# Kernel optimization log

Hardware: AMD Instinct MI355X
Metric: run time of the kernel (lower is better)

Reference implementation:

```python
import jax, jax.numpy as jnp
import numpy as np

NUM_EXPERTS = 8
TOP_K = 2


def setup_inputs() -> dict:
    key = jax.random.key(0)
    k0, k1, k2, k3, k4 = jax.random.split(key, 5)
    sl, bs, hs, ffn = 2048, 2, 512, 2048
    T = sl * bs
    x = jax.random.normal(k0, (sl, bs, hs), jnp.float32)
    expert_weights = jax.random.uniform(k1, (T, TOP_K), jnp.float32)
    expert_indices = jax.random.randint(k2, (T, TOP_K), 0, NUM_EXPERTS)
    # per-expert MLP params (ParallelGroupedMLP, 'regular' mlp_type)
    w1 = jax.random.normal(k3, (NUM_EXPERTS, hs, ffn), jnp.float32) * (hs ** -0.5)
    w2 = jax.random.normal(k4, (NUM_EXPERTS, ffn, hs), jnp.float32) * (ffn ** -0.5)
    return dict(x=x, expert_weights=expert_weights, expert_indices=expert_indices, w1=w1, w2=w2)


def reference(x, expert_weights, expert_indices, w1, w2):
    """Dropless MoE: sort assignments by expert, gather tokens, grouped MLP,
    scatter-combine with top-k router weights (megablocks gather/scatter semantics)."""
    in_shape = x.shape
    hs = in_shape[-1]
    x_flat = x.reshape(-1, hs)                 # [T, hs]
    T = x_flat.shape[0]
    flat_ids = expert_indices.reshape(-1)      # [T*k] expert id per assignment
    order = jnp.argsort(flat_ids)              # indices: assignment order sorted by expert
    bin_ids = flat_ids[order]                  # expert id per sorted slot
    token_ids = order // TOP_K                 # source token per sorted slot
    xg = x_flat[token_ids]                     # gather: [T*k, hs]
    # grouped GEMM: fixed small loop over experts, mask-select per slot
    y = jnp.zeros_like(xg)
    for e in range(NUM_EXPERTS):
        h = jax.nn.gelu(xg @ w1[e], approximate=False)   # [T*k, ffn]
        y = jnp.where((bin_ids == e)[:, None], h @ w2[e], y)
    # scatter-combine: out[token] += weight[assignment] * y[slot]
    w = expert_weights.reshape(-1)[order][:, None]       # [T*k, 1]
    out = jnp.zeros((T, hs), x.dtype).at[token_ids].add(w * y)
    return out.reshape(in_shape)
```

## Files before the change

kernel.cpp:

```cpp
#include <hip/hip_runtime.h>
#include <stdint.h>

#define T_TOK 4096
#define KTOP  2
#define HS    512
#define FFN   2048
#define NE    8
#define NA    (T_TOK*KTOP)
#define MT    128
#define BK    64
#define MT_MAX 72
#define SLOT_CAP (MT_MAX*MT)
#define PSTR 68
#define NB_G1 1152

#define MB_ (1024ull*1024ull)
#define WS_OFF   1024u
#define WS_MEXP  1088u
#define WS_SLOTS 2048u
#define WS_INV   40960u
#define WS_XB   (1*MB_)
#define WS_W1T  (5*MB_)
#define WS_W2T  (21*MB_)
#define WS_HB   (37*MB_)
#define WS_YPB0 (73*MB_)
#define WS_YPB1 (82*MB_)
#define WS_NEED (91*MB_)

typedef short bf16x8 __attribute__((ext_vector_type(8)));
typedef float f32x4  __attribute__((ext_vector_type(4)));

__device__ __forceinline__ unsigned short f2bf(float f) {
    unsigned u = __builtin_bit_cast(unsigned, f);
    u += 0x7fffu + ((u >> 16) & 1u);
    return (unsigned short)(u >> 16);
}
__device__ __forceinline__ float bf2f(unsigned short h) {
    return __builtin_bit_cast(float, (unsigned)h << 16);
}
__device__ __forceinline__ float gelu_fast(float x) {
    float x2 = x * x;
    float inner = fmaf(0.044715f * x2, x, x);
    float E = __expf(1.5957691216057308f * inner);
    return x - x / (1.0f + E);
}
__device__ __forceinline__ void gl_lds16(const void* g, void* l) {
    __builtin_amdgcn_global_load_lds(
        (const __attribute__((address_space(1))) unsigned int*)g,
        (__attribute__((address_space(3))) unsigned int*)l, 16, 0, 0);
}

__device__ __forceinline__ void transpose_cvt64(
    const float* __restrict__ src, unsigned short* __restrict__ dh,
    int R, int C, int e, int kb, int nb, int t, float (*tile)[65])
{
    const int k0 = kb * 64, n0 = nb * 64;
    #pragma unroll
    for (int q = 0; q < 4; ++q) {
        int f4 = t + q * 256;
        int kk = f4 >> 4, nn4 = f4 & 15;
        float4 v = *reinterpret_cast<const float4*>(
            &src[((size_t)e * R + k0 + kk) * C + n0 + nn4 * 4]);
        tile[kk][nn4 * 4 + 0] = v.x; tile[kk][nn4 * 4 + 1] = v.y;
        tile[kk][nn4 * 4 + 2] = v.z; tile[kk][nn4 * 4 + 3] = v.w;
    }
    __syncthreads();
    #pragma unroll
    for (int q = 0; q < 4; ++q) {
        int wid = t + q * 256;
        int nn = wid >> 4, kk4 = wid & 15;
        ushort4 o;
        o.x = f2bf(tile[kk4 * 4 + 0][nn]);
        o.y = f2bf(tile[kk4 * 4 + 1][nn]);
        o.z = f2bf(tile[kk4 * 4 + 2][nn]);
        o.w = f2bf(tile[kk4 * 4 + 3][nn]);
        *reinterpret_cast<ushort4*>(&dh[((size_t)e * C + n0 + nn) * R + k0 + kk4 * 4]) = o;
    }
}

__global__ void moe_prep1(const int* __restrict__ eidx,
                          int* slots, int* inv, int* offp, int* mexp,
                          const float* __restrict__ x, unsigned short* __restrict__ xb,
                          const float* __restrict__ w1, unsigned short* __restrict__ w1t)
{
    __shared__ float tile[64][65];
    const int bid = blockIdx.x, t = threadIdx.x;
    if (bid < 2048) {
        int i = bid * 256 + t;
        float4 v = reinterpret_cast<const float4*>(x)[i];
        uint2 p = { (unsigned)f2bf(v.x) | ((unsigned)f2bf(v.y) << 16),
                    (unsigned)f2bf(v.z) | ((unsigned)f2bf(v.w) << 16) };
        reinterpret_cast<uint2*>(xb)[i] = p;
    } else if (bid < 4096) {
        int lin = bid - 2048, e = lin >> 8, rem = lin & 255;
        transpose_cvt64(w1, w1t, HS, FFN, e, rem & 7, rem >> 3, t, tile);
    } else {
        __shared__ int hfull[NE], hpre[NE], elocal[256];
        __shared__ int off_l[NE + 1];
        const int f = bid - 4096;
        if (t < NE) { hfull[t] = 0; hpre[t] = 0; }
        __syncthreads();
        const int base = f * 256;
        for (int i = t; i < NA; i += 256) {
            int ee = eidx[i];
            atomicAdd(&hfull[ee], 1);
            if (i < base) atomicAdd(&hpre[ee], 1);
        }
        if (f < 32) elocal[t] = eidx[base + t];
        __syncthreads();
        if (t == 0) {
            int run = 0;
            for (int q = 0; q < NE; ++q) { off_l[q] = run; run += ((hfull[q] + MT - 1) / MT) * MT; }
            off_l[NE] = run;
        }
        __syncthreads();
        if (f < 32) {
            int a = base + t, e = elocal[t];
            int rank = 0;
            for (int j = 0; j < t; ++j) rank += (elocal[j] == e) ? 1 : 0;
            int s = off_l[e] + hpre[e] + rank;
            slots[s] = a;
            inv[a] = s;
        } else {
            for (int e = 0; e < NE; ++e)
                for (int s = off_l[e] + hfull[e] + t; s < off_l[e + 1]; s += 256)
                    slots[s] = -1;
            for (int s = off_l[NE] + t; s < SLOT_CAP; s += 256) slots[s] = -1;
            if (t <= NE) offp[t] = off_l[t];
            if (t < MT_MAX) {
                int m0 = t * MT, ee = 0;
                #pragma unroll
                for (int q = 0; q < NE; ++q)
                    if (m0 >= off_l[q] && m0 < off_l[q + 1]) ee = q;
                mexp[t] = ee;
            }
        }
    }
}

__global__ __launch_bounds__(256, 4) void moe_g1w2(
    const unsigned short* __restrict__ XB, const unsigned short* __restrict__ W1T,
    const int* __restrict__ offp, const int* __restrict__ mexp,
    const int* __restrict__ slots, unsigned short* __restrict__ HB,
    const float* __restrict__ w2, unsigned short* __restrict__ w2t)
{
    __shared__ __align__(16) char POOL[MT * PSTR * 4];
    __shared__ int srow[MT];
    const int t = threadIdx.x;

    if (blockIdx.x >= NB_G1) {
        int lin = blockIdx.x - NB_G1;
        int e = lin >> 8, rem = lin & 255;
        transpose_cvt64(w2, w2t, FFN, HS, e, rem & 31, rem >> 5, t,
                        reinterpret_cast<float(*)[65]>(POOL));
        return;
    }

    const int xcd = blockIdx.x & 7;
    const int part = blockIdx.x >> 3;
    const int mtg = part % 9;
    const int nt  = part / 9;
    const int mt  = xcd * 9 + mtg;
    if (mt * MT >= offp[NE]) return;
    const int e = mexp[mt];
    const int lane = t & 63, wv = t >> 6;

    short* As = (short*)POOL;
    short* Bs = (short*)(POOL + 16384);
    float* Pf = (float*)POOL;

    if (t < MT) { int s = slots[mt * MT + t]; srow[t] = (s < 0) ? 0 : (s >> 1); }
    __syncthreads();

    int baseA[4], baseB[4];
    #pragma unroll
    for (int q = 0; q < 4; ++q) {
        int i = wv * 4 + q;
        int row = i * 8 + (lane >> 3);
        int sg = (lane & 7) ^ (row & 7);
        baseA[q] = srow[row] * HS + sg * 8;
        baseB[q] = (e * FFN + nt * MT + row) * HS + sg * 8;
    }

    const int wm = wv >> 1, wn = wv & 1, q4 = lane >> 4, l15 = lane & 15;
    int offA[2][4], offB[2][4];
    #pragma unroll
    for (int m = 0; m < 4; ++m) {
        int r  = wm * 64 + m * 16 + l15;
        int rb = wn * 64 + m * 16 + l15;
        #pragma unroll
        for (int ks = 0; ks < 2; ++ks) {
            offA[ks][m] = r  * 128 + ((((ks << 2) | q4) ^ (r  & 7)) << 4);
            offB[ks][m] = rb * 128 + ((((ks << 2) | q4) ^ (rb & 7)) << 4);
        }
    }

    f32x4 acc[4][4];
    #pragma unroll
    for (int m = 0; m < 4; ++m)
        #pragma unroll
        for (int n = 0; n < 4; ++n) { f32x4 z = {0.f, 0.f, 0.f, 0.f}; acc[m][n] = z; }

    for (int kk = 0; kk < HS; kk += BK) {
        __syncthreads();
        #pragma unroll
        for (int q = 0; q < 4; ++q) {
            int i = wv * 4 + q;
            gl_lds16(XB  + baseA[q] + kk, (char*)As + i * 1024);
            gl_lds16(W1T + baseB[q] + kk, (char*)Bs + i * 1024);
        }
        __syncthreads();
        #pragma unroll
        for (int ks = 0; ks < 2; ++ks) {
            bf16x8 a[4], b[4];
            #pragma unroll
            for (int m = 0; m < 4; ++m) {
                a[m] = *(const bf16x8*)((const char*)As + offA[ks][m]);
                b[m] = *(const bf16x8*)((const char*)Bs + offB[ks][m]);
            }
            #pragma unroll
            for (int m = 0; m < 4; ++m)
                #pragma unroll
                for (int n = 0; n < 4; ++n)
                    acc[m][n] = __builtin_amdgcn_mfma_f32_16x16x32_bf16(a[m], b[n], acc[m][n], 0, 0, 0);
        }
    }

    #pragma unroll
    for (int half = 0; half < 2; ++half) {
        __syncthreads();
        if (wn == half) {
            #pragma unroll
            for (int m = 0; m < 4; ++m)
                #pragma unroll
                for (int n = 0; n < 4; ++n)
                    #pragma unroll
                    for (int j = 0; j < 4; ++j)
                        Pf[(wm * 64 + m * 16 + q4 * 4 + j) * PSTR + n * 16 + l15] = acc[m][n][j];
        }
        __syncthreads();
        #pragma unroll
        for (int q = 0; q < 4; ++q) {
            int seg = q * 256 + t, row = seg >> 3, c8 = (seg & 7) << 3;
            const float* p = Pf + row * PSTR + c8;
            float4 a = *(const float4*)p, b = *(const float4*)(p + 4);
            float va[8] = {a.x, a.y, a.z, a.w, b.x, b.y, b.z, b.w};
            bf16x8 ph;
            #pragma unroll
            for (int i = 0; i < 8; ++i) ph[i] = (short)f2bf(gelu_fast(va[i]));
            *(bf16x8*)(HB + (size_t)(mt * MT + row) * FFN + nt * MT + half * 64 + c8) = ph;
        }
    }
}

__global__ __launch_bounds__(256, 4) void moe_gemm2(
    const unsigned short* __restrict__ HB, const unsigned short* __restrict__ W2T,
    const int* __restrict__ offp, const int* __restrict__ mexp,
    unsigned short* __restrict__ YPB0, unsigned short* __restrict__ YPB1)
{
    const int xcd = blockIdx.x & 7;
    const int part = blockIdx.x >> 3;
    const int sub = part % 8;
    const int mtg = part / 8;
    const int mt  = xcd * 9 + mtg;
    const int nt  = sub >> 1, kpart = sub & 1;
    if (mt * MT >= offp[NE]) return;
    const int e = mexp[mt];
    const int t = threadIdx.x, lane = t & 63, wv = t >> 6;

    __shared__ __align__(16) char POOL[MT * PSTR * 4];
    short* As = (short*)POOL;
    short* Bs = (short*)(POOL + 16384);
    float* Pf = (float*)POOL;

    int baseA[4], baseB[4];
    #pragma unroll
    for (int q = 0; q < 4; ++q) {
        int i = wv * 4 + q;
        int row = i * 8 + (lane >> 3);
        int sg = (lane & 7) ^ (row & 7);
        baseA[q] = (mt * MT + row) * FFN + sg * 8;
        baseB[q] = (e * HS + nt * MT + row) * FFN + sg * 8;
    }

    const int wm = wv >> 1, wn = wv & 1, q4 = lane >> 4, l15 = lane & 15;
    int offA[2][4], offB[2][4];
    #pragma unroll
    for (int m = 0; m < 4; ++m) {
        int r  = wm * 64 + m * 16 + l15;
        int rb = wn * 64 + m * 16 + l15;
        #pragma unroll
        for (int ks = 0; ks < 2; ++ks) {
            offA[ks][m] = r  * 128 + ((((ks << 2) | q4) ^ (r  & 7)) << 4);
            offB[ks][m] = rb * 128 + ((((ks << 2) | q4) ^ (rb & 7)) << 4);
        }
    }

    f32x4 acc[4][4];
    #pragma unroll
    for (int m = 0; m < 4; ++m)
        #pragma unroll
        for (int n = 0; n < 4; ++n) { f32x4 z = {0.f, 0.f, 0.f, 0.f}; acc[m][n] = z; }

    const int k0 = kpart * (FFN / 2), k1 = k0 + FFN / 2;
    for (int kk = k0; kk < k1; kk += BK) {
        __syncthreads();
        #pragma unroll
        for (int q = 0; q < 4; ++q) {
            int i = wv * 4 + q;
            gl_lds16(HB  + baseA[q] + kk, (char*)As + i * 1024);
            gl_lds16(W2T + baseB[q] + kk, (char*)Bs + i * 1024);
        }
        __syncthreads();
        #pragma unroll
        for (int ks = 0; ks < 2; ++ks) {
            bf16x8 a[4], b[4];
            #pragma unroll
            for (int m = 0; m < 4; ++m) {
                a[m] = *(const bf16x8*)((const char*)As + offA[ks][m]);
                b[m] = *(const bf16x8*)((const char*)Bs + offB[ks][m]);
            }
            #pragma unroll
            for (int m = 0; m < 4; ++m)
                #pragma unroll
                for (int n = 0; n < 4; ++n)
                    acc[m][n] = __builtin_amdgcn_mfma_f32_16x16x32_bf16(a[m], b[n], acc[m][n], 0, 0, 0);
        }
    }

    unsigned short* YP = kpart ? YPB1 : YPB0;
    #pragma unroll
    for (int half = 0; half < 2; ++half) {
        __syncthreads();
        if (wn == half) {
            #pragma unroll
            for (int m = 0; m < 4; ++m)
                #pragma unroll
                for (int n = 0; n < 4; ++n)
                    #pragma unroll
                    for (int j = 0; j < 4; ++j)
                        Pf[(wm * 64 + m * 16 + q4 * 4 + j) * PSTR + n * 16 + l15] = acc[m][n][j];
        }
        __syncthreads();
        #pragma unroll
        for (int q = 0; q < 4; ++q) {
            int seg = q * 256 + t, row = seg >> 3, c8 = (seg & 7) << 3;
            const float* p = Pf + row * PSTR + c8;
            float4 a = *(const float4*)p, b = *(const float4*)(p + 4);
            float va[8] = {a.x, a.y, a.z, a.w, b.x, b.y, b.z, b.w};
            bf16x8 ph;
            #pragma unroll
            for (int i = 0; i < 8; ++i) ph[i] = (short)f2bf(va[i]);
            *(bf16x8*)(YP + (size_t)(mt * MT + row) * HS + nt * MT + half * 64 + c8) = ph;
        }
    }
}

__global__ void moe_combine2(const unsigned short* __restrict__ YPB0,
                             const unsigned short* __restrict__ YPB1,
                             const int* __restrict__ inv, const float* __restrict__ ew,
                             float* __restrict__ out) {
    int i = blockIdx.x * 256 + threadIdx.x;
    if (i >= T_TOK * HS / 8) return;
    int tk = i >> 6, c8 = (i & 63) << 3;
    int s0 = inv[2 * tk], s1 = inv[2 * tk + 1];
    float w0 = ew[2 * tk], w1 = ew[2 * tk + 1];
    bf16x8 a0 = *(const bf16x8*)(YPB0 + (size_t)s0 * HS + c8);
    bf16x8 b0 = *(const bf16x8*)(YPB1 + (size_t)s0 * HS + c8);
    bf16x8 a1 = *(const bf16x8*)(YPB0 + (size_t)s1 * HS + c8);
    bf16x8 b1 = *(const bf16x8*)(YPB1 + (size_t)s1 * HS + c8);
    float o[8];
    #pragma unroll
    for (int j = 0; j < 8; ++j)
        o[j] = w0 * (bf2f((unsigned short)a0[j]) + bf2f((unsigned short)b0[j]))
             + w1 * (bf2f((unsigned short)a1[j]) + bf2f((unsigned short)b1[j]));
    float4* d = reinterpret_cast<float4*>(out + (size_t)i * 8);
    d[0] = make_float4(o[0], o[1], o[2], o[3]);
    d[1] = make_float4(o[4], o[5], o[6], o[7]);
}

#define FB_BM 32
#define FB_BJ 128
#define FB_CK 256
#define FB_XSTR (FB_CK+4)
#define FB_HSTR (FB_BJ+4)

__device__ __forceinline__ float fb_gelu(float v) {
    return 0.5f * v * (1.0f + erff(v * 0.70710678118654752f));
}

__global__ void fb_init(int* cnt) { int i = threadIdx.x; if (i < NE) cnt[i] = 0; }

__global__ void fb_scatter(const int* __restrict__ eidx, int* cnt, int* bucket) {
    int a = blockIdx.x * 256 + threadIdx.x;
    if (a < NA) { int e = eidx[a]; int p = atomicAdd(&cnt[e], 1); bucket[e * NA + p] = a; }
}

__global__ __launch_bounds__(256, 1) void fb_fused(
    const float* __restrict__ x, const float* __restrict__ w1, const float* __restrict__ w2,
    const int* __restrict__ cnt, const int* __restrict__ bucket, float* __restrict__ ybuf)
{
    const int bid = blockIdx.x;
    const int e = bid & (NE - 1), tr = bid >> 3;
    const int n_e = cnt[e], rbase = tr * FB_BM;
    if (rbase >= n_e) return;
    const int t = threadIdx.x;
    __shared__ __align__(16) float Xc[FB_BM][FB_XSTR];
    __shared__ __align__(16) float Hsh[FB_BM][FB_HSTR];
    __shared__ int rowa[FB_BM];
    if (t < FB_BM) { int r = rbase + t; rowa[t] = (r < n_e) ? bucket[e * NA + r] : -1; }
    __syncthreads();
    const int cg = t & 15, rg = t >> 4, r0 = rg * 2;
    float yac[2][32];
    #pragma unroll
    for (int u = 0; u < 2; ++u)
        #pragma unroll
        for (int v = 0; v < 32; ++v) yac[u][v] = 0.0f;
    const float* w1e = w1 + (size_t)e * HS * FFN;
    const float* w2e = w2 + (size_t)e * FFN * HS;
    for (int jp = 0; jp < FFN; jp += FB_BJ) {
        float hac[2][8];
        #pragma unroll
        for (int u = 0; u < 2; ++u)
            #pragma unroll
            for (int v = 0; v < 8; ++v) hac[u][v] = 0.0f;
        for (int ic = 0; ic < HS; ic += FB_CK) {
            __syncthreads();
            #pragma unroll
            for (int q = 0; q < (FB_BM * FB_CK / 4) / 256; ++q) {
                int id = t + 256 * q, rr = id >> 6, c4 = id & 63;
                int a = rowa[rr];
                float4 val = make_float4(0.f, 0.f, 0.f, 0.f);
                if (a >= 0) val = *reinterpret_cast<const float4*>(x + (size_t)(a >> 1) * HS + ic + c4 * 4);
                *reinterpret_cast<float4*>(&Xc[rr][c4 * 4]) = val;
            }
            __syncthreads();
            const float* w1p = w1e + (size_t)ic * FFN + jp + cg * 8;
            #pragma unroll 2
            for (int i4 = 0; i4 < FB_CK; i4 += 4) {
                float4 xa = *reinterpret_cast<const float4*>(&Xc[r0][i4]);
                float4 xb = *reinterpret_cast<const float4*>(&Xc[r0 + 1][i4]);
                const float* wr0 = w1p + (size_t)i4 * FFN;
                #pragma unroll
                for (int ii = 0; ii < 4; ++ii) {
                    float4 wa = *reinterpret_cast<const float4*>(wr0 + (size_t)ii * FFN);
                    float4 wb = *reinterpret_cast<const float4*>(wr0 + (size_t)ii * FFN + 4);
                    float x0 = (ii == 0) ? xa.x : (ii == 1) ? xa.y : (ii == 2) ? xa.z : xa.w;
                    float x1 = (ii == 0) ? xb.x : (ii == 1) ? xb.y : (ii == 2) ? xb.z : xb.w;
                    hac[0][0] = fmaf(x0, wa.x, hac[0][0]); hac[0][1] = fmaf(x0, wa.y, hac[0][1]);
                    hac[0][2] = fmaf(x0, wa.z, hac[0][2]); hac[0][3] = fmaf(x0, wa.w, hac[0][3]);
                    hac[0][4] = fmaf(x0, wb.x, hac[0][4]); hac[0][5] = fmaf(x0, wb.y, hac[0][5]);
                    hac[0][6] = fmaf(x0, wb.z, hac[0][6]); hac[0][7] = fmaf(x0, wb.w, hac[0][7]);
                    hac[1][0] = fmaf(x1, wa.x, hac[1][0]); hac[1][1] = fmaf(x1, wa.y, hac[1][1]);
                    hac[1][2] = fmaf(x1, wa.z, hac[1][2]); hac[1][3] = fmaf(x1, wa.w, hac[1][3]);
                    hac[1][4] = fmaf(x1, wb.x, hac[1][4]); hac[1][5] = fmaf(x1, wb.y, hac[1][5]);
                    hac[1][6] = fmaf(x1, wb.z, hac[1][6]); hac[1][7] = fmaf(x1, wb.w, hac[1][7]);
                }
            }
        }
        #pragma unroll
        for (int u = 0; u < 2; ++u)
            #pragma unroll
            for (int v = 0; v < 8; ++v) Hsh[r0 + u][cg * 8 + v] = fb_gelu(hac[u][v]);
        __syncthreads();
        const float* w2p = w2e + (size_t)jp * HS + cg * 32;
        #pragma unroll 2
        for (int j = 0; j < FB_BJ; ++j) {
            float h0 = Hsh[r0][j], h1 = Hsh[r0 + 1][j];
            const float* wr = w2p + (size_t)j * HS;
            #pragma unroll
            for (int q = 0; q < 8; ++q) {
                float4 w4 = *reinterpret_cast<const float4*>(wr + q * 4);
                yac[0][q * 4 + 0] = fmaf(h0, w4.x, yac[0][q * 4 + 0]);
                yac[0][q * 4 + 1] = fmaf(h0, w4.y, yac[0][q * 4 + 1]);
                yac[0][q * 4 + 2] = fmaf(h0, w4.z, yac[0][q * 4 + 2]);
                yac[0][q * 4 + 3] = fmaf(h0, w4.w, yac[0][q * 4 + 3]);
                yac[1][q * 4 + 0] = fmaf(h1, w4.x, yac[1][q * 4 + 0]);
                yac[1][q * 4 + 1] = fmaf(h1, w4.y, yac[1][q * 4 + 1]);
                yac[1][q * 4 + 2] = fmaf(h1, w4.z, yac[1][q * 4 + 2]);
                yac[1][q * 4 + 3] = fmaf(h1, w4.w, yac[1][q * 4 + 3]);
            }
        }
    }
    #pragma unroll
    for (int u = 0; u < 2; ++u) {
        int a = rowa[r0 + u];
        if (a >= 0) {
            float* yp = ybuf + (size_t)a * HS + cg * 32;
            #pragma unroll
            for (int q = 0; q < 8; ++q) {
                float4 o = make_float4(yac[u][q * 4 + 0], yac[u][q * 4 + 1],
                                       yac[u][q * 4 + 2], yac[u][q * 4 + 3]);
                *reinterpret_cast<float4*>(yp + q * 4) = o;
            }
        }
    }
}

__global__ void fb_combine(const float* __restrict__ ybuf, const float* __restrict__ ew,
                           float* __restrict__ out) {
    int i = blockIdx.x * 256 + threadIdx.x;
    if (i >= T_TOK * HS / 4) return;
    int tk = i >> 7, c4 = i & 127;
    float wA = ew[2 * tk], wB = ew[2 * tk + 1];
    const float4* y4 = reinterpret_cast<const float4*>(ybuf);
    float4 a = y4[(size_t)(2 * tk) * (HS / 4) + c4];
    float4 b = y4[(size_t)(2 * tk + 1) * (HS / 4) + c4];
    float4 o;
    o.x = wA * a.x + wB * b.x; o.y = wA * a.y + wB * b.y;
    o.z = wA * a.z + wB * b.z; o.w = wA * a.w + wB * b.w;
    reinterpret_cast<float4*>(out)[i] = o;
}

extern "C" void kernel_launch(void* const* d_in, const int* in_sizes, int n_in,
                              void* d_out, int out_size, void* d_ws, size_t ws_size,
                              hipStream_t stream) {
    const float* x  = (const float*)d_in[0];
    const float* ew = (const float*)d_in[1];
    const int*   ei = (const int*)d_in[2];
    const float* w1 = (const float*)d_in[3];
    const float* w2 = (const float*)d_in[4];
    float* out = (float*)d_out;
    char* W = (char*)d_ws;

    if (ws_size < WS_NEED) {
        int* cnt = (int*)d_ws;
        int* bucket = cnt + 64;
        float* ybuf = (float*)(W + (1 << 19));
        fb_init<<<1, 64, 0, stream>>>(cnt);
        fb_scatter<<<NA / 256, 256, 0, stream>>>(ei, cnt, bucket);
        fb_fused<<<NE * (NA / FB_BM), 256, 0, stream>>>(x, w1, w2, cnt, bucket, ybuf);
        fb_combine<<<(T_TOK * HS / 4 + 255) / 256, 256, 0, stream>>>(ybuf, ew, out);
        return;
    }

    int* offp  = (int*)(W + WS_OFF);
    int* mexp  = (int*)(W + WS_MEXP);
    int* slots = (int*)(W + WS_SLOTS);
    int* inv   = (int*)(W + WS_INV);
    unsigned short* XB   = (unsigned short*)(W + WS_XB);
    unsigned short* W1T  = (unsigned short*)(W + WS_W1T);
    unsigned short* W2T  = (unsigned short*)(W + WS_W2T);
    unsigned short* HB   = (unsigned short*)(W + WS_HB);
    unsigned short* YPB0 = (unsigned short*)(W + WS_YPB0);
    unsigned short* YPB1 = (unsigned short*)(W + WS_YPB1);

    moe_prep1<<<4129, 256, 0, stream>>>(ei, slots, inv, offp, mexp, x, XB, w1, W1T);
    moe_g1w2<<<NB_G1 + 2048, 256, 0, stream>>>(XB, W1T, offp, mexp, slots, HB, w2, W2T);
    moe_gemm2<<<8 * 9 * 8, 256, 0, stream>>>(HB, W2T, offp, mexp, YPB0, YPB1);
    moe_combine2<<<(T_TOK * HS / 8) / 256, 256, 0, stream>>>(YPB0, YPB1, inv, ew, out);
}
```

Baseline: 96.66 us.

## Widen GEMM1 N-tile to 256 columns per block for better A reuse

```diff
diff --git a/kernel.cpp b/kernel.cpp
--- a/kernel.cpp
+++ b/kernel.cpp
@@ -12,7 +12,7 @@
 #define MT_MAX 72
 #define SLOT_CAP (MT_MAX*MT)
 #define PSTR 68
-#define NB_G1 1152
+#define NB_G1 576
 
 #define MB_ (1024ull*1024ull)
 #define WS_OFF   1024u
@@ -138,13 +138,13 @@
     }
 }
 
-__global__ __launch_bounds__(256, 4) void moe_g1w2(
+__global__ __launch_bounds__(256, 2) void moe_g1w2(
     const unsigned short* __restrict__ XB, const unsigned short* __restrict__ W1T,
     const int* __restrict__ offp, const int* __restrict__ mexp,
     const int* __restrict__ slots, unsigned short* __restrict__ HB,
     const float* __restrict__ w2, unsigned short* __restrict__ w2t)
 {
-    __shared__ __align__(16) char POOL[MT * PSTR * 4];
+    __shared__ __align__(16) char POOL[49152];
     __shared__ int srow[MT];
     const int t = threadIdx.x;
 
@@ -172,71 +172,83 @@
     if (t < MT) { int s = slots[mt * MT + t]; srow[t] = (s < 0) ? 0 : (s >> 1); }
     __syncthreads();
 
-    int baseA[4], baseB[4];
+    int baseA[4], baseB[8];
     #pragma unroll
     for (int q = 0; q < 4; ++q) {
         int i = wv * 4 + q;
         int row = i * 8 + (lane >> 3);
         int sg = (lane & 7) ^ (row & 7);
         baseA[q] = srow[row] * HS + sg * 8;
-        baseB[q] = (e * FFN + nt * MT + row) * HS + sg * 8;
+    }
+    #pragma unroll
+    for (int q = 0; q < 8; ++q) {
+        int j = wv * 8 + q;
+        int row = j * 8 + (lane >> 3);
+        int sg = (lane & 7) ^ (row & 7);
+        baseB[q] = (e * FFN + nt * 256 + row) * HS + sg * 8;
     }
 
     const int wm = wv >> 1, wn = wv & 1, q4 = lane >> 4, l15 = lane & 15;
-    int offA[2][4], offB[2][4];
+    int offA[2][4], offB[2][8];
     #pragma unroll
     for (int m = 0; m < 4; ++m) {
-        int r  = wm * 64 + m * 16 + l15;
-        int rb = wn * 64 + m * 16 + l15;
+        int r = wm * 64 + m * 16 + l15;
+        #pragma unroll
+        for (int ks = 0; ks < 2; ++ks)
+            offA[ks][m] = r * 128 + ((((ks << 2) | q4) ^ (r & 7)) << 4);
+    }
+    #pragma unroll
+    for (int n = 0; n < 8; ++n) {
+        int rb = wn * 128 + n * 16 + l15;
+        #pragma unroll
+        for (int ks = 0; ks < 2; ++ks)
+            offB[ks][n] = rb * 128 + ((((ks << 2) | q4) ^ (rb & 7)) << 4);
+    }
+
+    f32x4 acc[4][8];
+    #pragma unroll
+    for (int m = 0; m < 4; ++m)
+        #pragma unroll
+        for (int n = 0; n < 8; ++n) { f32x4 z = {0.f, 0.f, 0.f, 0.f}; acc[m][n] = z; }
+
+    for (int kk = 0; kk < HS; kk += BK) {
+        __syncthreads();
+        #pragma unroll
+        for (int q = 0; q < 4; ++q)
+            gl_lds16(XB + baseA[q] + kk, (char*)As + (wv * 4 + q) * 1024);
+        #pragma unroll
+        for (int q = 0; q < 8; ++q)
+            gl_lds16(W1T + baseB[q] + kk, (char*)Bs + (wv * 8 + q) * 1024);
+        __syncthreads();
         #pragma unroll
         for (int ks = 0; ks < 2; ++ks) {
-            offA[ks][m] = r  * 128 + ((((ks << 2) | q4) ^ (r  & 7)) << 4);
-            offB[ks][m] = rb * 128 + ((((ks << 2) | q4) ^ (rb & 7)) << 4);
-        }
-    }
-
-    f32x4 acc[4][4];
-    #pragma unroll
-    for (int m = 0; m < 4; ++m)
-        #pragma unroll
-        for (int n = 0; n < 4; ++n) { f32x4 z = {0.f, 0.f, 0.f, 0.f}; acc[m][n] = z; }
-
-    for (int kk = 0; kk < HS; kk += BK) {
-        __syncthreads();
-        #pragma unroll
-        for (int q = 0; q < 4; ++q) {
-            int i = wv * 4 + q;
-            gl_lds16(XB  + baseA[q] + kk, (char*)As + i * 1024);
-            gl_lds16(W1T + baseB[q] + kk, (char*)Bs + i * 1024);
-        }
-        __syncthreads();
-        #pragma unroll
-        for (int ks = 0; ks < 2; ++ks) {
-            bf16x8 a[4], b[4];
-            #pragma unroll
-            for (int m = 0; m < 4; ++m) {
+            bf16x8 a[4], b[8];
+            #pragma unroll
+            for (int m = 0; m < 4; ++m)
                 a[m] = *(const bf16x8*)((const char*)As + offA[ks][m]);
-                b[m] = *(const bf16x8*)((const char*)Bs + offB[ks][m]);
-            }
+            #pragma unroll
+            for (int n = 0; n < 8; ++n)
+                b[n] = *(const bf16x8*)((const char*)Bs + offB[ks][n]);
             #pragma unroll
             for (int m = 0; m < 4; ++m)
                 #pragma unroll
-                for (int n = 0; n < 4; ++n)
+                for (int n = 0; n < 8; ++n)
                     acc[m][n] = __builtin_amdgcn_mfma_f32_16x16x32_bf16(a[m], b[n], acc[m][n], 0, 0, 0);
         }
     }
 
     #pragma unroll
-    for (int half = 0; half < 2; ++half) {
-        __syncthreads();
-        if (wn == half) {
+    for (int qq = 0; qq < 4; ++qq) {
+        const int wn_q = qq >> 1, nq = (qq & 1) * 4;
+        __syncthreads();
+        if (wn == wn_q) {
             #pragma unroll
             for (int m = 0; m < 4; ++m)
                 #pragma unroll
-                for (int n = 0; n < 4; ++n)
+                for (int nn = 0; nn < 4; ++nn)
                     #pragma unroll
                     for (int j = 0; j < 4; ++j)
-                        Pf[(wm * 64 + m * 16 + q4 * 4 + j) * PSTR + n * 16 + l15] = acc[m][n][j];
+                        Pf[(wm * 64 + m * 16 + q4 * 4 + j) * PSTR + nn * 16 + l15] = acc[m][nq + nn][j];
         }
         __syncthreads();
         #pragma unroll
@@ -248,7 +260,7 @@
             bf16x8 ph;
             #pragma unroll
             for (int i = 0; i < 8; ++i) ph[i] = (short)f2bf(gelu_fast(va[i]));
-            *(bf16x8*)(HB + (size_t)(mt * MT + row) * FFN + nt * MT + half * 64 + c8) = ph;
+            *(bf16x8*)(HB + (size_t)(mt * MT + row) * FFN + nt * 256 + qq * 64 + c8) = ph;
         }
     }
 }
```

Measured after the change: 101.8 us. 5.3% more time.
